# Performance work log

Hardware: AMD Instinct MI355X
Metric: run time of the kernel (lower is better)

## Reference

```python
import jax, jax.numpy as jnp
import numpy as np

DIM, NH, T_MAX = 1024, 16, 2048
HD = DIM // NH
EPS = 1e-6


def _rope_tables(T, hd, dtype=jnp.float32):
    inv_freq = 1.0 / (10000.0 ** (jnp.arange(0, hd, 2, dtype=jnp.float32) / hd))
    t = jnp.arange(T, dtype=jnp.float32)
    freqs = jnp.outer(t, inv_freq)                 # [T, hd/2]
    emb = jnp.concatenate([freqs, freqs], axis=-1)  # [T, hd]
    return jnp.cos(emb).astype(dtype), jnp.sin(emb).astype(dtype)


def _rotate_half(x):
    x1, x2 = jnp.split(x, 2, axis=-1)
    return jnp.concatenate([-x2, x1], axis=-1)


def _rmsnorm(x, g):
    rms = jnp.sqrt(jnp.mean(x * x, axis=-1, keepdims=True) + EPS)
    return x / rms * g


def setup_inputs() -> dict:
    key = jax.random.key(0)
    ks = jax.random.split(key, 10)
    B, T, C = 4, 2048, DIM
    s = 1.0 / np.sqrt(C)
    x = jax.random.normal(ks[0], (B, T, C), dtype=jnp.float32)
    mask = jnp.tril(jnp.ones((T, T), dtype=jnp.int32))[None, None, :, :]
    wq = jax.random.normal(ks[1], (C, C), jnp.float32) * s
    wk = jax.random.normal(ks[2], (C, C), jnp.float32) * s
    wv = jax.random.normal(ks[3], (C, C), jnp.float32) * s
    wo = jax.random.normal(ks[4], (C, C), jnp.float32) * s
    w1 = jax.random.normal(ks[5], (C, 4 * C), jnp.float32) * s
    w2 = jax.random.normal(ks[6], (4 * C, C), jnp.float32) * (1.0 / np.sqrt(4 * C))
    w3 = jax.random.normal(ks[7], (C, 4 * C), jnp.float32) * s
    g1 = jnp.ones((C,), jnp.float32)
    g2 = jnp.ones((C,), jnp.float32)
    return {"x": x, "mask": mask, "g1": g1, "wq": wq, "wk": wk, "wv": wv,
            "wo": wo, "g2": g2, "w1": w1, "w2": w2, "w3": w3}


def reference(x, mask, g1, wq, wk, wv, wo, g2, w1, w2, w3):
    B, T, C = x.shape
    scale = HD ** -0.5
    # --- attention sublayer ---
    h = _rmsnorm(x, g1)
    q = (h @ wq).reshape(B, T, NH, HD)
    k = (h @ wk).reshape(B, T, NH, HD)
    v = (h @ wv).reshape(B, T, NH, HD)
    cos, sin = _rope_tables(T, HD, x.dtype)
    cos = cos[None, :, None, :]
    sin = sin[None, :, None, :]
    q = q * cos + _rotate_half(q) * sin
    k = k * cos + _rotate_half(k) * sin
    attn = jnp.einsum("bthd,bshd->bhts", q, k) * scale  # [B,H,T,T]
    attn = jnp.where(mask == 0, -jnp.inf, attn)
    attn = jax.nn.softmax(attn, axis=-1)
    o = jnp.einsum("bhts,bshd->bthd", attn, v).reshape(B, T, C)
    x = x + o @ wo
    # --- SwiGLU FFN sublayer ---
    h = _rmsnorm(x, g2)
    x = x + (jax.nn.silu(h @ w1) * (h @ w3)) @ w2
    return x
```

## Files before the change

### kernel.cpp

```cpp
#include <hip/hip_runtime.h>
#include <cstdint>

typedef unsigned short u16;
typedef __attribute__((ext_vector_type(8))) short bf16x8;
typedef __attribute__((ext_vector_type(4))) float f32x4;

__device__ __forceinline__ u16 f2b(float f) {
  union { float f; unsigned u; } c; c.f = f;
  unsigned u = c.u;
  return (u16)((u + 0x7FFFu + ((u >> 16) & 1u)) >> 16);
}
__device__ __forceinline__ float b2f(u16 b) {
  union { unsigned u; float f; } c; c.u = ((unsigned)b) << 16;
  return c.f;
}

typedef __attribute__((address_space(1))) void gv_t;
typedef __attribute__((address_space(3))) void lv_t;
__device__ __forceinline__ void gload_lds16(const void* g, void* l) {
  __builtin_amdgcn_global_load_lds((gv_t*)g, (lv_t*)l, 16, 0, 0);
}

__global__ void transpose_f2b(const float* __restrict__ in, u16* __restrict__ out,
                              int R, int C) {
  __shared__ float t[32][33];
  const int c0 = blockIdx.x * 32, r0 = blockIdx.y * 32;
  const int tx = threadIdx.x, ty = threadIdx.y;
#pragma unroll
  for (int i = 0; i < 4; ++i)
    t[ty + 8 * i][tx] = in[(size_t)(r0 + ty + 8 * i) * C + c0 + tx];
  __syncthreads();
#pragma unroll
  for (int i = 0; i < 4; ++i)
    out[(size_t)(c0 + ty + 8 * i) * R + r0 + tx] = f2b(t[tx][ty + 8 * i]);
}

__global__ __launch_bounds__(256) void rmsnorm_k(const float* __restrict__ x,
                                                 const float* __restrict__ g,
                                                 u16* __restrict__ out) {
  const int row = blockIdx.x, tid = threadIdx.x;
  const float4 v = ((const float4*)x)[(size_t)row * 256 + tid];
  float ss = v.x * v.x + v.y * v.y + v.z * v.z + v.w * v.w;
#pragma unroll
  for (int off = 1; off < 64; off <<= 1) ss += __shfl_xor(ss, off, 64);
  __shared__ float red[4];
  if ((tid & 63) == 0) red[tid >> 6] = ss;
  __syncthreads();
  const float mean = (red[0] + red[1] + red[2] + red[3]) * (1.0f / 1024.0f);
  const float rinv = 1.0f / sqrtf(mean + 1e-6f);
  const float4 gv = ((const float4*)g)[tid];
  u16* o = out + (size_t)row * 1024 + tid * 4;
  o[0] = f2b(v.x * rinv * gv.x);
  o[1] = f2b(v.y * rinv * gv.y);
  o[2] = f2b(v.z * rinv * gv.z);
  o[3] = f2b(v.w * rinv * gv.w);
}

__global__ __launch_bounds__(256) void rope_k(u16* __restrict__ qkv) {
  const int i = blockIdx.x * 256 + threadIdx.x;
  const int d = i & 31;
  const int h = (i >> 5) & 15;
  const int bt = i >> 9;
  const int t = bt & 2047;
  const float inv = exp2f((float)d * -0.4152410118609203f);
  const float th = (float)t * inv;
  float s, c;
  sincosf(th, &s, &c);
  size_t base = (size_t)bt * 3072 + h * 64 + d;
#pragma unroll
  for (int half = 0; half < 2; ++half) {
    const float x1 = b2f(qkv[base]);
    const float x2 = b2f(qkv[base + 32]);
    qkv[base]      = f2b(x1 * c - x2 * s);
    qkv[base + 32] = f2b(x2 * c + x1 * s);
    base += 1024;
  }
}

__global__ void vtrans_k(const u16* __restrict__ qkv, u16* __restrict__ VT) {
  __shared__ u16 tl[32][34];
  const int t0 = blockIdx.x * 32;
  const int bh = blockIdx.y >> 1;
  const int d0 = (blockIdx.y & 1) * 32;
  const int b = bh >> 4, h = bh & 15;
  const int tx = threadIdx.x, ty = threadIdx.y;
  const u16* src = qkv + (size_t)(b * 2048 + t0) * 3072 + 2048 + h * 64 + d0;
#pragma unroll
  for (int i = 0; i < 4; ++i)
    tl[ty + 8 * i][tx] = src[(size_t)(ty + 8 * i) * 3072 + tx];
  __syncthreads();
  u16* dst = VT + ((size_t)bh * 64 + d0) * 2048 + t0;
#pragma unroll
  for (int i = 0; i < 4; ++i)
    dst[(size_t)(ty + 8 * i) * 2048 + tx] = tl[tx][ty + 8 * i];
}

template <int EPI>
__global__ __launch_bounds__(256)
void gemm_bt(const u16* __restrict__ A, const u16* __restrict__ BT,
             void* __restrict__ Cout, const float* __restrict__ resid,
             int M, int N, int K, int lda) {
  __shared__ alignas(16) u16 As[128 * 32];
  __shared__ alignas(16) u16 Bs[128 * 32];
  const int tid = threadIdx.x;
  const int wave = tid >> 6, lane = tid & 63;
  const int wr = wave >> 1, wc = wave & 1;
  const int l15 = lane & 15, quad = lane >> 4;
  const int bm = blockIdx.x * 128, bn = blockIdx.y * 128;

  f32x4 acc[4][4];
#pragma unroll
  for (int i = 0; i < 4; ++i)
#pragma unroll
    for (int j = 0; j < 4; ++j) acc[i][j] = (f32x4){0.f, 0.f, 0.f, 0.f};

  const int srow = wave * 32 + (lane >> 2);
  const int scol = (lane & 3) * 8;
  const u16* gA0 = A + (size_t)(bm + srow) * lda + scol;
  const u16* gA1 = gA0 + (size_t)16 * lda;
  const u16* gB0 = BT + (size_t)(bn + srow) * K + scol;
  const u16* gB1 = gB0 + (size_t)16 * K;
  u16* lA0 = As + wave * 1024; u16* lA1 = lA0 + 512;
  u16* lB0 = Bs + wave * 1024; u16* lB1 = lB0 + 512;

  const u16* pa = As + (wr * 64 + l15) * 32 + quad * 8;
  const u16* pb = Bs + (wc * 64 + l15) * 32 + quad * 8;

  for (int kt = 0; kt < K; kt += 32) {
    gload_lds16(gA0 + kt, lA0);
    gload_lds16(gA1 + kt, lA1);
    gload_lds16(gB0 + kt, lB0);
    gload_lds16(gB1 + kt, lB1);
    __syncthreads();
    bf16x8 af[4], bfv[4];
#pragma unroll
    for (int i = 0; i < 4; ++i) af[i] = *(const bf16x8*)(pa + i * 512);
#pragma unroll
    for (int j = 0; j < 4; ++j) bfv[j] = *(const bf16x8*)(pb + j * 512);
#pragma unroll
    for (int i = 0; i < 4; ++i)
#pragma unroll
      for (int j = 0; j < 4; ++j)
        acc[i][j] = __builtin_amdgcn_mfma_f32_16x16x32_bf16(af[i], bfv[j], acc[i][j], 0, 0, 0);
    __syncthreads();
  }

#pragma unroll
  for (int i = 0; i < 4; ++i) {
    const int gr = bm + wr * 64 + i * 16 + quad * 4;
#pragma unroll
    for (int j = 0; j < 4; ++j) {
      const int gc = bn + wc * 64 + j * 16 + l15;
#pragma unroll
      for (int r = 0; r < 4; ++r) {
        const size_t off = (size_t)(gr + r) * N + gc;
        if (EPI == 0) {
          ((u16*)Cout)[off] = f2b(acc[i][j][r]);
        } else {
          ((float*)Cout)[off] = resid[off] + acc[i][j][r];
        }
      }
    }
  }
}

template <int EPI>
__global__ __launch_bounds__(512, 2)
void gemm256(const u16* __restrict__ A, const u16* __restrict__ BT,
             void* __restrict__ Cout, const float* __restrict__ resid,
             int M, int N, int K, int lda) {
  __shared__ alignas(16) u16 LDS[65536];
  char* const ldsc = (char*)LDS;
  const int tid = threadIdx.x;
  const int wave = tid >> 6, lane = tid & 63;
  const int wr = wave >> 2, wc = wave & 3;
  const int l15 = lane & 15, quad = lane >> 4;
  const int bm = blockIdx.x * 256, bn = blockIdx.y * 256;
  const int NT = K >> 6;
  const int NIT = NT >> 1;

  const int swz = (l15 & 8) << 2;
  const int aoff = (((wr * 64 + l15) * 64 + quad * 16) ^ swz);
  const int boff = (((wc * 32 + l15) * 64 + quad * 16) ^ swz) + 65536;

  const int kperm = ((lane & 3) ^ ((lane >> 5) << 1)) * 8;
  const u16* sA = A + (size_t)(bm + wave * 16 + (lane >> 2)) * lda + kperm;
  const u16* sB = BT + (size_t)(bn + wave * 16 + (lane >> 2)) * K + kperm;
  const size_t hA = (size_t)128 * lda;
  const size_t hB = (size_t)128 * K;
  const int dstW = wave * 1024;

  f32x4 acc[8][4];
#pragma unroll
  for (int m = 0; m < 8; ++m)
#pragma unroll
    for (int n = 0; n < 4; ++n) acc[m][n] = (f32x4){0.f, 0.f, 0.f, 0.f};
  bf16x8 a[4][2], b[2][2];

#define STAGE(kt_, slot_, buf_)                                               \
  if ((kt_) < NT) {                                                           \
    const u16* s_ = (((slot_) & 1) ? sB + ((size_t)((slot_) >> 1)) * hB       \
                                   : sA + ((size_t)((slot_) >> 1)) * hA) +    \
                    (size_t)(kt_) * 64;                                       \
    char* d_ = ldsc + (((slot_) & 1) ? 65536 : 0) + (buf_) * 32768 +          \
               ((slot_) >> 1) * 16384 + dstW;                                 \
    gload_lds16(s_, d_);                                                      \
    gload_lds16(s_ + 32, d_ + 8192);                                          \
  }

#define LOAD_A(mh_, buf_)                                                     \
  _Pragma("unroll") for (int mf = 0; mf < 4; ++mf)                            \
      _Pragma("unroll") for (int kk = 0; kk < 2; ++kk)                        \
          a[mf][kk] = *(const bf16x8*)(ldsc + aoff + (buf_) * 32768 +         \
                                       (mh_) * 16384 + kk * 8192 + mf * 1024);

#define LOAD_B(nh_, buf_)                                                     \
  _Pragma("unroll") for (int nf = 0; nf < 2; ++nf)                            \
      _Pragma("unroll") for (int kk = 0; kk < 2; ++kk)                        \
          b[nf][kk] = *(const bf16x8*)(ldsc + boff + (buf_) * 32768 +         \
                                       (nh_) * 16384 + kk * 8192 + nf * 1024);

#define MMA(mh_, nh_)                                                         \
  __builtin_amdgcn_s_setprio(1);                                              \
  _Pragma("unroll") for (int mf = 0; mf < 4; ++mf)                            \
      _Pragma("unroll") for (int nf = 0; nf < 2; ++nf)                        \
          _Pragma("unroll") for (int kk = 0; kk < 2; ++kk)                    \
              acc[(mh_) * 4 + mf][(nh_) * 2 + nf] =                           \
                  __builtin_amdgcn_mfma_f32_16x16x32_bf16(                    \
                      a[mf][kk], b[nf][kk],                                   \
                      acc[(mh_) * 4 + mf][(nh_) * 2 + nf], 0, 0, 0);          \
  __builtin_amdgcn_s_setprio(0);

#define BAR() __builtin_amdgcn_s_barrier()
#define DRAIN_LGKM()                                                          \
  {                                                                           \
    asm volatile("s_waitcnt lgkmcnt(0)" ::: "memory");                        \
    __builtin_amdgcn_sched_barrier(0);                                        \
  }

  STAGE(0, 0, 0); STAGE(0, 1, 0); STAGE(0, 2, 0); STAGE(0, 3, 0);
  STAGE(1, 0, 1); STAGE(1, 1, 1);
  asm volatile("s_waitcnt vmcnt(4)" ::: "memory");
  BAR();

  for (int i = 0; i < NIT; ++i) {
    const int t = 2 * i;
    LOAD_A(0, 0); LOAD_B(0, 0); STAGE(t + 1, 2, 1);
    BAR(); DRAIN_LGKM(); MMA(0, 0); BAR();
    LOAD_B(1, 0); STAGE(t + 1, 3, 1);
    BAR(); DRAIN_LGKM(); MMA(0, 1); BAR();
    LOAD_A(1, 0); LOAD_B(0, 0); STAGE(t + 2, 0, 0);
    BAR(); DRAIN_LGKM(); MMA(1, 0); BAR();
    LOAD_B(1, 0); STAGE(t + 2, 1, 0);
    BAR(); DRAIN_LGKM(); MMA(1, 1);
    if (i == NIT - 1) { asm volatile("s_waitcnt vmcnt(0)" ::: "memory"); }
    else              { asm volatile("s_waitcnt vmcnt(4)" ::: "memory"); }
    BAR();
    LOAD_A(0, 1); LOAD_B(0, 1); STAGE(t + 2, 2, 0);
    BAR(); DRAIN_LGKM(); MMA(0, 0); BAR();
    LOAD_B(1, 1); STAGE(t + 2, 3, 0);
    BAR(); DRAIN_LGKM(); MMA(0, 1); BAR();
    LOAD_A(1, 1); LOAD_B(0, 1); STAGE(t + 3, 0, 1);
    BAR(); DRAIN_LGKM(); MMA(1, 0); BAR();
    LOAD_B(1, 1); STAGE(t + 3, 1, 1);
    BAR(); DRAIN_LGKM(); MMA(1, 1);
    if (i < NIT - 1) { asm volatile("s_waitcnt vmcnt(4)" ::: "memory"); }
    BAR();
  }
#undef STAGE
#undef LOAD_A
#undef LOAD_B
#undef MMA
#undef BAR
#undef DRAIN_LGKM

#pragma unroll
  for (int m = 0; m < 8; ++m) {
    const int gr = bm + (m >> 2) * 128 + wr * 64 + (m & 3) * 16 + quad * 4;
#pragma unroll
    for (int n = 0; n < 4; ++n) {
      const int gc = bn + (n >> 1) * 128 + wc * 32 + (n & 1) * 16 + l15;
#pragma unroll
      for (int r = 0; r < 4; ++r) {
        const size_t off = (size_t)(gr + r) * N + gc;
        if (EPI == 0) {
          ((u16*)Cout)[off] = f2b(acc[m][n][r]);
        } else {
          ((float*)Cout)[off] = resid[off] + acc[m][n][r];
        }
      }
    }
  }
}

__global__ __launch_bounds__(256)
void attn_kernel(const u16* __restrict__ QKV, const u16* __restrict__ VT,
                 u16* __restrict__ O) {
  const int T = 2048, stQ = 3072;
  const int tid = threadIdx.x, wave = tid >> 6, lane = tid & 63;
  const int l15 = lane & 15, quad = lane >> 4;
  const int qt = (int)gridDim.x - 1 - (int)blockIdx.x;
  const int qb0 = qt * 128;
  const int bh = blockIdx.y, b = bh >> 4, h = bh & 15;
  const float sc2 = 0.125f * 1.44269504088896f;
  const float M0 = 32.0f;

  __shared__ alignas(16) u16 Kf[2][8 * 512];
  __shared__ alignas(16) u16 Vf[2][8 * 512];
  __shared__ alignas(16) u16 Pl[4][2][16 * 72];

  const u16* Qb  = QKV + (size_t)b * T * stQ + h * 64;
  const u16* Kb  = Qb + 1024;
  const u16* VTb = VT + (size_t)bh * 64 * T;

  const int r0 = qb0 + wave * 16;
  const int r1 = r0 + 64;
  const u16* qp0 = Qb + (size_t)(r0 + l15) * stQ + quad * 8;
  const u16* qp1 = Qb + (size_t)(r1 + l15) * stQ + quad * 8;
  const bf16x8 qf00 = *(const bf16x8*)qp0;
  const bf16x8 qf01 = *(const bf16x8*)(qp0 + 32);
  const bf16x8 qf10 = *(const bf16x8*)qp1;
  const bf16x8 qf11 = *(const bf16x8*)(qp1 + 32);

  bf16x8 ones;
#pragma unroll
  for (int j = 0; j < 8; ++j) ones[j] = (short)0x3F80;

  const u16* kS = Kb + (size_t)(wave * 16 + l15) * stQ + quad * 8;
  const u16* vS = VTb + (size_t)(wave * 16 + l15) * T + quad * 8;

  f32x4 o0[4], o1[4], sum0, sum1;
#pragma unroll
  for (int c = 0; c < 4; ++c) {
    o0[c] = (f32x4){0.f, 0.f, 0.f, 0.f};
    o1[c] = (f32x4){0.f, 0.f, 0.f, 0.f};
  }
  sum0 = (f32x4){0.f, 0.f, 0.f, 0.f};
  sum1 = (f32x4){0.f, 0.f, 0.f, 0.f};

  u16* pw0 = &Pl[wave][0][0];
  u16* pw1 = &Pl[wave][1][0];

  const int nkt = qt * 2 + 2;

  gload_lds16(kS,      &Kf[0][(wave * 2 + 0) * 512]);
  gload_lds16(kS + 32, &Kf[0][(wave * 2 + 1) * 512]);
  gload_lds16(vS,      &Vf[0][(wave * 2 + 0) * 512]);
  gload_lds16(vS + 32, &Vf[0][(wave * 2 + 1) * 512]);

  for (int kt = 0; kt < nkt; ++kt) {
    const int kb0 = kt * 64;
    const int buf = kt & 1;
    __builtin_amdgcn_sched_barrier(0);
    if (kt + 1 < nkt) {
      const size_t kb1 = (size_t)(kb0 + 64);
      gload_lds16(kS + kb1 * stQ,      &Kf[buf ^ 1][(wave * 2 + 0) * 512]);
      gload_lds16(kS + kb1 * stQ + 32, &Kf[buf ^ 1][(wave * 2 + 1) * 512]);
      gload_lds16(vS + kb1,            &Vf[buf ^ 1][(wave * 2 + 0) * 512]);
      gload_lds16(vS + kb1 + 32,       &Vf[buf ^ 1][(wave * 2 + 1) * 512]);
      asm volatile("s_waitcnt vmcnt(4)" ::: "memory");
    } else {
      asm volatile("s_waitcnt vmcnt(0)" ::: "memory");
    }
    __builtin_amdgcn_s_barrier();
    __builtin_amdgcn_sched_barrier(0);

    bf16x8 kf[8], vf[8];
#pragma unroll
    for (int g = 0; g < 8; ++g) {
      kf[g] = *(const bf16x8*)(&Kf[buf][g * 512 + lane * 8]);
      vf[g] = *(const bf16x8*)(&Vf[buf][g * 512 + lane * 8]);
    }

    const bool act0 = (kb0 <= r0 + 15);

    {
      f32x4 s[4];
      __builtin_amdgcn_s_setprio(1);
#pragma unroll
      for (int jj = 0; jj < 4; ++jj) {
        s[jj] = (f32x4){0.f, 0.f, 0.f, 0.f};
        s[jj] = __builtin_amdgcn_mfma_f32_16x16x32_bf16(qf10, kf[jj * 2 + 0], s[jj], 0, 0, 0);
        s[jj] = __builtin_amdgcn_mfma_f32_16x16x32_bf16(qf11, kf[jj * 2 + 1], s[jj], 0, 0, 0);
      }
      __builtin_amdgcn_s_setprio(0);
      if (kb0 + 63 > r1) {
#pragma unroll
        for (int jj = 0; jj < 4; ++jj)
#pragma unroll
          for (int r = 0; r < 4; ++r) {
            const bool msk = (kb0 + jj * 16 + l15) > (r1 + quad * 4 + r);
            const float a = msk ? -1e30f : (s[jj][r] * sc2 - M0);
            pw1[(quad * 4 + r) * 72 + jj * 16 + l15] = f2b(exp2f(a));
          }
      } else {
#pragma unroll
        for (int jj = 0; jj < 4; ++jj)
#pragma unroll
          for (int r = 0; r < 4; ++r)
            pw1[(quad * 4 + r) * 72 + jj * 16 + l15] =
                f2b(exp2f(s[jj][r] * sc2 - M0));
      }
    }
    if (act0) {
      f32x4 s[4];
      __builtin_amdgcn_s_setprio(1);
#pragma unroll
      for (int jj = 0; jj < 4; ++jj) {
        s[jj] = (f32x4){0.f, 0.f, 0.f, 0.f};
        s[jj] = __builtin_amdgcn_mfma_f32_16x16x32_bf16(qf00, kf[jj * 2 + 0], s[jj], 0, 0, 0);
        s[jj] = __builtin_amdgcn_mfma_f32_16x16x32_bf16(qf01, kf[jj * 2 + 1], s[jj], 0, 0, 0);
      }
      __builtin_amdgcn_s_setprio(0);
      if (kb0 + 63 > r0) {
#pragma unroll
        for (int jj = 0; jj < 4; ++jj)
#pragma unroll
          for (int r = 0; r < 4; ++r) {
            const bool msk = (kb0 + jj * 16 + l15) > (r0 + quad * 4 + r);
            const float a = msk ? -1e30f : (s[jj][r] * sc2 - M0);
            pw0[(quad * 4 + r) * 72 + jj * 16 + l15] = f2b(exp2f(a));
          }
      } else {
#pragma unroll
        for (int jj = 0; jj < 4; ++jj)
#pragma unroll
          for (int r = 0; r < 4; ++r)
            pw0[(quad * 4 + r) * 72 + jj * 16 + l15] =
                f2b(exp2f(s[jj][r] * sc2 - M0));
      }
    }

    const bf16x8 pf10 = *(const bf16x8*)(pw1 + l15 * 72 + quad * 8);
    const bf16x8 pf11 = *(const bf16x8*)(pw1 + l15 * 72 + 32 + quad * 8);
    __builtin_amdgcn_s_setprio(1);
#pragma unroll
    for (int c = 0; c < 4; ++c) {
      o1[c] = __builtin_amdgcn_mfma_f32_16x16x32_bf16(pf10, vf[c * 2 + 0], o1[c], 0, 0, 0);
      o1[c] = __builtin_amdgcn_mfma_f32_16x16x32_bf16(pf11, vf[c * 2 + 1], o1[c], 0, 0, 0);
    }
    sum1 = __builtin_amdgcn_mfma_f32_16x16x32_bf16(pf10, ones, sum1, 0, 0, 0);
    sum1 = __builtin_amdgcn_mfma_f32_16x16x32_bf16(pf11, ones, sum1, 0, 0, 0);
    __builtin_amdgcn_s_setprio(0);
    if (act0) {
      const bf16x8 pf00 = *(const bf16x8*)(pw0 + l15 * 72 + quad * 8);
      const bf16x8 pf01 = *(const bf16x8*)(pw0 + l15 * 72 + 32 + quad * 8);
      __builtin_amdgcn_s_setprio(1);
#pragma unroll
      for (int c = 0; c < 4; ++c) {
        o0[c] = __builtin_amdgcn_mfma_f32_16x16x32_bf16(pf00, vf[c * 2 + 0], o0[c], 0, 0, 0);
        o0[c] = __builtin_amdgcn_mfma_f32_16x16x32_bf16(pf01, vf[c * 2 + 1], o0[c], 0, 0, 0);
      }
      sum0 = __builtin_amdgcn_mfma_f32_16x16x32_bf16(pf00, ones, sum0, 0, 0, 0);
      sum0 = __builtin_amdgcn_mfma_f32_16x16x32_bf16(pf01, ones, sum0, 0, 0, 0);
      __builtin_amdgcn_s_setprio(0);
    }
    __builtin_amdgcn_s_barrier();
  }

  float i0[4], i1[4];
#pragma unroll
  for (int r = 0; r < 4; ++r) { i0[r] = 1.f / sum0[r]; i1[r] = 1.f / sum1[r]; }
  u16* op0 = O + ((size_t)(b * T) + r0 + quad * 4) * 1024 + h * 64 + l15;
  u16* op1 = O + ((size_t)(b * T) + r1 + quad * 4) * 1024 + h * 64 + l15;
#pragma unroll
  for (int c = 0; c < 4; ++c)
#pragma unroll
    for (int r = 0; r < 4; ++r) {
      op0[(size_t)r * 1024 + c * 16] = f2b(o0[c][r] * i0[r]);
      op1[(size_t)r * 1024 + c * 16] = f2b(o1[c][r] * i1[r]);
    }
}

__global__ __launch_bounds__(256) void gate_k(u16* __restrict__ a13) {
  const size_t i = (size_t)blockIdx.x * 256 + threadIdx.x;
  const size_t row = i >> 9, c8 = (i & 511) * 8;
  u16* p1v = a13 + row * 8192 + c8;
  const u16* p3v = p1v + 4096;
  uint4 u1 = *(uint4*)p1v;
  const uint4 u3 = *(const uint4*)p3v;
  u16* p1 = (u16*)&u1;
  const u16* p3 = (const u16*)&u3;
#pragma unroll
  for (int j = 0; j < 8; ++j) {
    const float a = b2f(p1[j]);
    const float g = b2f(p3[j]);
    const float s = a / (1.f + __expf(-a));
    p1[j] = f2b(s * g);
  }
  *(uint4*)p1v = u1;
}

extern "C" void kernel_launch(void* const* d_in, const int* in_sizes, int n_in,
                              void* d_out, int out_size, void* d_ws, size_t ws_size,
                              hipStream_t stream) {
  const float* x  = (const float*)d_in[0];
  const float* g1 = (const float*)d_in[2];
  const float* wq = (const float*)d_in[3];
  const float* wk = (const float*)d_in[4];
  const float* wv = (const float*)d_in[5];
  const float* wo = (const float*)d_in[6];
  const float* g2 = (const float*)d_in[7];
  const float* w1 = (const float*)d_in[8];
  const float* w2 = (const float*)d_in[9];
  const float* w3 = (const float*)d_in[10];
  float* out = (float*)d_out;

  const int T = 2048, NH = 16, B = 4;
  const int M = B * T;
  const size_t MB = 1ull << 20;

  char* ws = (char*)d_ws;
  u16* hb    = (u16*)(ws);
  u16* wqkvT = (u16*)(ws + 16 * MB);
  u16* woT   = (u16*)(ws + 22 * MB);
  u16* w13T  = (u16*)(ws + 24 * MB);
  u16* w2T   = (u16*)(ws + 40 * MB);
  u16* qkv   = (u16*)(ws + 48 * MB);
  u16* VT    = (u16*)(ws + 96 * MB);
  u16* Ob    = (u16*)(ws + 112 * MB);
  u16* a13   = (u16*)(ws + 48 * MB);

  const dim3 tb(32, 8);
  transpose_f2b<<<dim3(32, 32),  tb, 0, stream>>>(wq, wqkvT,              1024, 1024);
  transpose_f2b<<<dim3(32, 32),  tb, 0, stream>>>(wk, wqkvT + 1024*1024,  1024, 1024);
  transpose_f2b<<<dim3(32, 32),  tb, 0, stream>>>(wv, wqkvT + 2048*1024,  1024, 1024);
  transpose_f2b<<<dim3(32, 32),  tb, 0, stream>>>(wo, woT, 1024, 1024);
  transpose_f2b<<<dim3(128, 32), tb, 0, stream>>>(w1, w13T,               1024, 4096);
  transpose_f2b<<<dim3(128, 32), tb, 0, stream>>>(w3, w13T + 4096*1024,   1024, 4096);
  transpose_f2b<<<dim3(32, 128), tb, 0, stream>>>(w2, w2T, 4096, 1024);

  rmsnorm_k<<<M, 256, 0, stream>>>(x, g1, hb);

  gemm256<0><<<dim3(32, 12), 512, 0, stream>>>(hb, wqkvT, qkv, nullptr, M, 3072, 1024, 1024);

  rope_k<<<16384, 256, 0, stream>>>(qkv);
  vtrans_k<<<dim3(64, 128), tb, 0, stream>>>(qkv, VT);

  attn_kernel<<<dim3(T / 128, B * NH), 256, 0, stream>>>(qkv, VT, Ob);

  gemm_bt<1><<<dim3(64, 8), 256, 0, stream>>>(Ob, woT, out, x, M, 1024, 1024, 1024);

  rmsnorm_k<<<M, 256, 0, stream>>>(out, g2, hb);

  gemm256<0><<<dim3(32, 32), 512, 0, stream>>>(hb, w13T, a13, nullptr, M, 8192, 1024, 1024);

  gate_k<<<16384, 256, 0, stream>>>(a13);

  gemm_bt<1><<<dim3(64, 8), 256, 0, stream>>>(a13, w2T, out, out, M, 1024, 4096, 8192);
}
```

Before: 723.1 us.

## Add 256x128 pipelined GEMM kernel for output and down projections

Introduces gemm256n, a 512-thread kernel with a 256x128 tile that uses direct global-to-LDS loads, double buffering, swizzled LDS and MFMA 16x16x32 bf16. It replaces gemm_bt for the wo projection and the w2 down projection, which have N=1024. The aim is more operand reuse per block and overlap of loads with MFMA work on these narrow-N GEMMs. The trade-off is fewer blocks (256) on the device and a hand-tuned waitcnt schedule that has to be correct for its accuracy to hold.

Result: faster. 693.5 us (-4.1%).

```diff
diff --git a/kernel.cpp b/kernel.cpp
--- a/kernel.cpp
+++ b/kernel.cpp
@@ -271,15 +271,134 @@
 #undef LOAD_A
 #undef LOAD_B
 #undef MMA
+
+#pragma unroll
+  for (int m = 0; m < 8; ++m) {
+    const int gr = bm + (m >> 2) * 128 + wr * 64 + (m & 3) * 16 + quad * 4;
+#pragma unroll
+    for (int n = 0; n < 4; ++n) {
+      const int gc = bn + (n >> 1) * 128 + wc * 32 + (n & 1) * 16 + l15;
+#pragma unroll
+      for (int r = 0; r < 4; ++r) {
+        const size_t off = (size_t)(gr + r) * N + gc;
+        if (EPI == 0) {
+          ((u16*)Cout)[off] = f2b(acc[m][n][r]);
+        } else {
+          ((float*)Cout)[off] = resid[off] + acc[m][n][r];
+        }
+      }
+    }
+  }
 #undef BAR
 #undef DRAIN_LGKM
+}
+
+template <int EPI>
+__global__ __launch_bounds__(512, 2)
+void gemm256n(const u16* __restrict__ A, const u16* __restrict__ BT,
+              void* __restrict__ Cout, const float* __restrict__ resid,
+              int M, int N, int K, int lda) {
+  __shared__ alignas(16) u16 LDS[49152];
+  char* const ldsc = (char*)LDS;
+  const int tid = threadIdx.x;
+  const int wave = tid >> 6, lane = tid & 63;
+  const int wr = wave >> 2, wc = wave & 3;
+  const int l15 = lane & 15, quad = lane >> 4;
+  const int bm = blockIdx.x * 256, bn = blockIdx.y * 128;
+  const int NT = K >> 6;
+
+  const int swz = (l15 & 8) << 2;
+  const int aoff = (((wr * 64 + l15) * 64 + quad * 16) ^ swz);
+  const int boff = (((wc * 32 + l15) * 64 + quad * 16) ^ swz) + 65536;
+
+  const int kperm = ((lane & 3) ^ ((lane >> 5) << 1)) * 8;
+  const u16* sA = A + (size_t)(bm + wave * 16 + (lane >> 2)) * lda + kperm;
+  const u16* sB = BT + (size_t)(bn + wave * 16 + (lane >> 2)) * K + kperm;
+  const size_t hA = (size_t)128 * lda;
+  const int dstW = wave * 1024;
+
+  f32x4 acc[8][2];
+#pragma unroll
+  for (int m = 0; m < 8; ++m)
+#pragma unroll
+    for (int n = 0; n < 2; ++n) acc[m][n] = (f32x4){0.f, 0.f, 0.f, 0.f};
+  bf16x8 a[4][2], b[2][2];
+
+#define STAGE_A(kt_, half_, buf_)                                             \
+  if ((kt_) < NT) {                                                           \
+    const u16* s_ = sA + (size_t)(half_) * hA + (size_t)(kt_) * 64;           \
+    char* d_ = ldsc + (buf_) * 32768 + (half_) * 16384 + dstW;                \
+    gload_lds16(s_, d_);                                                      \
+    gload_lds16(s_ + 32, d_ + 8192);                                          \
+  }
+#define STAGE_B(kt_, buf_)                                                    \
+  if ((kt_) < NT) {                                                           \
+    const u16* s_ = sB + (size_t)(kt_) * 64;                                  \
+    char* d_ = ldsc + 65536 + (buf_) * 16384 + dstW;                          \
+    gload_lds16(s_, d_);                                                      \
+    gload_lds16(s_ + 32, d_ + 8192);                                          \
+  }
+#define LOAD_A(mh_, buf_)                                                     \
+  _Pragma("unroll") for (int mf = 0; mf < 4; ++mf)                            \
+      _Pragma("unroll") for (int kk = 0; kk < 2; ++kk)                        \
+          a[mf][kk] = *(const bf16x8*)(ldsc + aoff + (buf_) * 32768 +         \
+                                       (mh_) * 16384 + kk * 8192 + mf * 1024);
+#define LOAD_B(buf_)                                                          \
+  _Pragma("unroll") for (int nf = 0; nf < 2; ++nf)                            \
+      _Pragma("unroll") for (int kk = 0; kk < 2; ++kk)                        \
+          b[nf][kk] = *(const bf16x8*)(ldsc + boff + (buf_) * 16384 +         \
+                                       kk * 8192 + nf * 1024);
+#define MMA(mh_)                                                              \
+  __builtin_amdgcn_s_setprio(1);                                              \
+  _Pragma("unroll") for (int mf = 0; mf < 4; ++mf)                            \
+      _Pragma("unroll") for (int nf = 0; nf < 2; ++nf)                        \
+          _Pragma("unroll") for (int kk = 0; kk < 2; ++kk)                    \
+              acc[(mh_) * 4 + mf][nf] =                                       \
+                  __builtin_amdgcn_mfma_f32_16x16x32_bf16(                    \
+                      a[mf][kk], b[nf][kk], acc[(mh_) * 4 + mf][nf], 0, 0, 0);\
+  __builtin_amdgcn_s_setprio(0);
+#define BAR() __builtin_amdgcn_s_barrier()
+#define DRAIN_LGKM()                                                          \
+  {                                                                           \
+    asm volatile("s_waitcnt lgkmcnt(0)" ::: "memory");                        \
+    __builtin_amdgcn_sched_barrier(0);                                        \
+  }
+
+  STAGE_A(0, 0, 0); STAGE_B(0, 0);
+  STAGE_A(0, 1, 0);
+  STAGE_A(1, 0, 1); STAGE_B(1, 1);
+  asm volatile("s_waitcnt vmcnt(6)" ::: "memory");
+  BAR();
+
+  for (int t = 0; t < NT; ++t) {
+    const int bsel = t & 1;
+    LOAD_A(0, bsel); LOAD_B(bsel);
+    STAGE_A(t + 1, 1, bsel ^ 1);
+    BAR(); DRAIN_LGKM(); MMA(0);
+    if (t == NT - 1) { asm volatile("s_waitcnt vmcnt(0)" ::: "memory"); }
+    else             { asm volatile("s_waitcnt vmcnt(6)" ::: "memory"); }
+    BAR();
+    LOAD_A(1, bsel);
+    STAGE_A(t + 2, 0, bsel); STAGE_B(t + 2, bsel);
+    BAR(); DRAIN_LGKM(); MMA(1);
+    if (t == NT - 2)     { asm volatile("s_waitcnt vmcnt(2)" ::: "memory"); }
+    else if (t < NT - 2) { asm volatile("s_waitcnt vmcnt(6)" ::: "memory"); }
+    BAR();
+  }
+#undef STAGE_A
+#undef STAGE_B
+#undef LOAD_A
+#undef LOAD_B
+#undef MMA
+#undef BAR
+#undef DRAIN_LGKM
 
 #pragma unroll
   for (int m = 0; m < 8; ++m) {
     const int gr = bm + (m >> 2) * 128 + wr * 64 + (m & 3) * 16 + quad * 4;
 #pragma unroll
-    for (int n = 0; n < 4; ++n) {
-      const int gc = bn + (n >> 1) * 128 + wc * 32 + (n & 1) * 16 + l15;
+    for (int n = 0; n < 2; ++n) {
+      const int gc = bn + wc * 32 + n * 16 + l15;
 #pragma unroll
       for (int r = 0; r < 4; ++r) {
         const size_t off = (size_t)(gr + r) * N + gc;
@@ -539,7 +658,7 @@
 
   attn_kernel<<<dim3(T / 128, B * NH), 256, 0, stream>>>(qkv, VT, Ob);
 
-  gemm_bt<1><<<dim3(64, 8), 256, 0, stream>>>(Ob, woT, out, x, M, 1024, 1024, 1024);
+  gemm256n<1><<<dim3(32, 8), 512, 0, stream>>>(Ob, woT, out, x, M, 1024, 1024, 1024);
 
   rmsnorm_k<<<M, 256, 0, stream>>>(out, g2, hb);
 
@@ -547,5 +666,5 @@
 
   gate_k<<<16384, 256, 0, stream>>>(a13);
 
-  gemm_bt<1><<<dim3(64, 8), 256, 0, stream>>>(a13, w2T, out, out, M, 1024, 4096, 8192);
-}
+  gemm256n<1><<<dim3(32, 8), 512, 0, stream>>>(a13, w2T, out, out, M, 1024, 4096, 8192);
+}
```
